# Kernel optimization log

Measured on AMD Instinct MI355X. Metric: run time of the kernel, lower is better.

The kernel has to match this reference:

```python
import jax, jax.numpy as jnp
import numpy as np

N, H, E = 50000, 128, 1600000

def setup_inputs() -> dict:
    key = jax.random.key(0)
    k1, k2, k3, k4 = jax.random.split(key, 4)
    h = jax.random.normal(k1, (N, H), dtype=jnp.float32)
    edge_index = jax.random.randint(k2, (2, E), 0, N, dtype=jnp.int64)
    # edge_scorer: Linear(2H, 1); node_scorer: Linear(H, 1)
    W_edge = jax.random.normal(k3, (2 * H, 1), dtype=jnp.float32) / np.sqrt(2 * H)
    b_edge = jnp.zeros((1,), dtype=jnp.float32)
    W_node = jax.random.normal(k4, (H, 1), dtype=jnp.float32) / np.sqrt(H)
    b_node = jnp.zeros((1,), dtype=jnp.float32)
    return {"h": h, "edge_index": edge_index, "W_edge": W_edge,
            "b_edge": b_edge, "W_node": W_node, "b_node": b_node}

def reference(h, edge_index, W_edge, b_edge, W_node, b_node):
    n = h.shape[0]
    src, dst = edge_index[0], edge_index[1]
    # cat([h[src], h[dst]]) @ W_edge == (h @ W_src)[src] + (h @ W_dst)[dst]
    # (same math as the torch module, avoids materializing the (E, 2H) concat)
    W_src, W_dst = W_edge[:h.shape[1]], W_edge[h.shape[1]:]
    s_src = (h @ W_src)[:, 0]            # (N,)
    s_dst = (h @ W_dst)[:, 0]            # (N,)
    edge_scores = s_src[src] + s_dst[dst] + b_edge[0]   # (E,)
    node_edge_score = jax.ops.segment_sum(edge_scores, dst, num_segments=n)
    node_self_score = (h @ W_node)[:, 0] + b_node[0]    # (N,)
    combined = node_edge_score + node_self_score
    return jax.nn.softmax(combined, axis=0)
```

## Files before the change

kernel.cpp:

```cpp
#include <hip/hip_runtime.h>
#include <math.h>


#define RANGE_BITS 14
#define RANGE_SIZE (1 << RANGE_BITS)
#define NCHUNKS 128
#define STAT_BLOCKS 256

typedef float vfloat4 __attribute__((ext_vector_type(4)));

__global__ __launch_bounds__(256) void node_scores_kernel(
    const float* __restrict__ h,
    const float* __restrict__ W_edge,
    const float* __restrict__ b_edge,
    const float* __restrict__ W_node,
    const float* __restrict__ b_node,
    float* __restrict__ s_src,
    float* __restrict__ t_dst,
    float* __restrict__ self_sc,
    float* __restrict__ acc,
    int N, int H)
{
    const int lane16 = threadIdx.x & 15;
    const int n = (blockIdx.x * blockDim.x + threadIdx.x) >> 4;
    if (n >= N) return;

    const float4* __restrict__ h4  = (const float4*)(h + (size_t)n * H);
    const float4* __restrict__ ws4 = (const float4*)(W_edge);
    const float4* __restrict__ wd4 = (const float4*)(W_edge + H);
    const float4* __restrict__ wn4 = (const float4*)(W_node);
    const int H4 = H >> 2;

    float ps = 0.0f, pd = 0.0f, pn = 0.0f;
    for (int i = lane16; i < H4; i += 16) {
        float4 hv = h4[i];
        float4 a = ws4[i], b = wd4[i], c = wn4[i];
        ps = fmaf(hv.x, a.x, fmaf(hv.y, a.y, fmaf(hv.z, a.z, fmaf(hv.w, a.w, ps))));
        pd = fmaf(hv.x, b.x, fmaf(hv.y, b.y, fmaf(hv.z, b.z, fmaf(hv.w, b.w, pd))));
        pn = fmaf(hv.x, c.x, fmaf(hv.y, c.y, fmaf(hv.z, c.z, fmaf(hv.w, c.w, pn))));
    }
    #pragma unroll
    for (int off = 8; off > 0; off >>= 1) {
        ps += __shfl_xor(ps, off, 64);
        pd += __shfl_xor(pd, off, 64);
        pn += __shfl_xor(pn, off, 64);
    }
    if (lane16 == 0) {
        float self = pn + b_node[0];
        s_src[n]   = ps;
        t_dst[n]   = pd + b_edge[0];
        self_sc[n] = self;
        acc[n]     = self;
    }
}

__global__ __launch_bounds__(1024) void edge_bin_kernel(
    const int* __restrict__ ei,
    const float* __restrict__ s_src,
    const float* __restrict__ t_dst,
    float* __restrict__ partials,
    int N, int E, int chunk, int vec_ok)
{
    __shared__ float hist[RANGE_SIZE];
    const int b  = blockIdx.x;
    const int r  = blockIdx.y;
    const int lo = r << RANGE_BITS;
    const int hi = min(lo + RANGE_SIZE, N);
    const unsigned span = (unsigned)(hi - lo);

    {
        vfloat4* __restrict__ hz = (vfloat4*)hist;
        const vfloat4 z = {0.0f, 0.0f, 0.0f, 0.0f};
        for (int i = threadIdx.x; i < (RANGE_SIZE >> 2); i += blockDim.x)
            hz[i] = z;
    }
    __syncthreads();

    const int e0 = b * chunk;
    const int e1 = min(e0 + chunk, E);
    if (e0 < e1) {
        if (vec_ok) {
            const int nvec = (e1 - e0) >> 2;
            const int4* __restrict__ dst4 = (const int4*)(ei + E + e0);
            const int4* __restrict__ src4 = (const int4*)(ei + e0);
            for (int i = threadIdx.x; i < nvec; i += blockDim.x) {
                int4 d = dst4[i];
                int4 s = src4[i];
                unsigned ux = (unsigned)(d.x - lo), uy = (unsigned)(d.y - lo);
                unsigned uz = (unsigned)(d.z - lo), uw = (unsigned)(d.w - lo);
                if (ux < span) atomicAdd(&hist[ux], s_src[s.x] + t_dst[d.x]);
                if (uy < span) atomicAdd(&hist[uy], s_src[s.y] + t_dst[d.y]);
                if (uz < span) atomicAdd(&hist[uz], s_src[s.z] + t_dst[d.z]);
                if (uw < span) atomicAdd(&hist[uw], s_src[s.w] + t_dst[d.w]);
            }
            for (int e = e0 + 4 * nvec + threadIdx.x; e < e1; e += blockDim.x) {
                int d = ei[E + e];
                unsigned u = (unsigned)(d - lo);
                if (u < span) atomicAdd(&hist[u], s_src[ei[e]] + t_dst[d]);
            }
        } else {
            for (int e = e0 + threadIdx.x; e < e1; e += blockDim.x) {
                int d = ei[E + e];
                unsigned u = (unsigned)(d - lo);
                if (u < span) atomicAdd(&hist[u], s_src[ei[e]] + t_dst[d]);
            }
        }
    }
    __syncthreads();

    float* __restrict__ outp = partials + (size_t)b * N + lo;
    const int len = hi - lo;
    if ((len & 3) == 0) {
        const int len4 = len >> 2;
        const vfloat4* __restrict__ h4 = (const vfloat4*)hist;
        vfloat4* __restrict__ o4 = (vfloat4*)outp;
        for (int i = threadIdx.x; i < len4; i += blockDim.x)
            __builtin_nontemporal_store(h4[i], &o4[i]);
    } else {
        for (int i = threadIdx.x; i < len; i += blockDim.x)
            __builtin_nontemporal_store(hist[i], &outp[i]);
    }
}

__global__ __launch_bounds__(256) void edge_accum_fallback_kernel(
    const int* __restrict__ ei,
    const float* __restrict__ s_src,
    const float* __restrict__ t_dst,
    float* __restrict__ acc,
    int E)
{
    int e = blockIdx.x * blockDim.x + threadIdx.x;
    if (e >= E) return;
    int s = ei[e];
    int d = ei[E + e];
    atomicAdd(&acc[d], s_src[s] + t_dst[d]);
}

__device__ __forceinline__ float blockReduceMaxB(float v) {
    __shared__ float sm[16];
    #pragma unroll
    for (int off = 32; off > 0; off >>= 1) v = fmaxf(v, __shfl_xor(v, off, 64));
    const int w = threadIdx.x >> 6, l = threadIdx.x & 63;
    const int nw = blockDim.x >> 6;
    if (l == 0) sm[w] = v;
    __syncthreads();
    float r = sm[0];
    for (int i = 1; i < nw; ++i) r = fmaxf(r, sm[i]);
    __syncthreads();
    return r;
}

__device__ __forceinline__ float blockReduceSumB(float v) {
    __shared__ float sm[16];
    #pragma unroll
    for (int off = 32; off > 0; off >>= 1) v += __shfl_xor(v, off, 64);
    const int w = threadIdx.x >> 6, l = threadIdx.x & 63;
    const int nw = blockDim.x >> 6;
    if (l == 0) sm[w] = v;
    __syncthreads();
    float r = 0.0f;
    for (int i = 0; i < nw; ++i) r += sm[i];
    __syncthreads();
    return r;
}

__global__ __launch_bounds__(256) void combine_stats_kernel(
    const float* __restrict__ self_sc,
    const float* __restrict__ partials,
    float* __restrict__ acc,
    float* __restrict__ red,
    int N, int B, int use_partials)
{
    float m = -INFINITY, l = 0.0f;
    for (int i = blockIdx.x * blockDim.x + threadIdx.x; i < N;
         i += gridDim.x * blockDim.x) {
        float v;
        if (use_partials) {
            float v0 = self_sc[i], v1 = 0.0f, v2 = 0.0f, v3 = 0.0f;
            int b = 0;
            for (; b + 4 <= B; b += 4) {
                v0 += __builtin_nontemporal_load(&partials[(size_t)(b + 0) * N + i]);
                v1 += __builtin_nontemporal_load(&partials[(size_t)(b + 1) * N + i]);
                v2 += __builtin_nontemporal_load(&partials[(size_t)(b + 2) * N + i]);
                v3 += __builtin_nontemporal_load(&partials[(size_t)(b + 3) * N + i]);
            }
            for (; b < B; ++b) v0 += partials[(size_t)b * N + i];
            v = (v0 + v1) + (v2 + v3);
            acc[i] = v;
        } else {
            v = acc[i];
        }
        float nm = fmaxf(m, v);
        l = l * __expf(m - nm) + __expf(v - nm);
        m = nm;
    }
    float mb = blockReduceMaxB(m);
    float ladj = (m == -INFINITY) ? 0.0f : l * __expf(m - mb);
    float lb = blockReduceSumB(ladj);
    if (threadIdx.x == 0) {
        red[blockIdx.x] = mb;
        red[STAT_BLOCKS + blockIdx.x] = lb;
    }
}

__global__ __launch_bounds__(256) void finalize_kernel(
    const float* __restrict__ acc,
    const float* __restrict__ red,
    float* __restrict__ out,
    int N)
{
    float m = red[threadIdx.x];
    float l = red[STAT_BLOCKS + threadIdx.x];
    float M = blockReduceMaxB(m);
    float L = blockReduceSumB(l * __expf(m - M));
    const float inv = 1.0f / L;

    int i = blockIdx.x * blockDim.x + threadIdx.x;
    if (i < N) out[i] = __expf(acc[i] - M) * inv;
}

extern "C" void kernel_launch(void* const* d_in, const int* in_sizes, int n_in,
                              void* d_out, int out_size, void* d_ws, size_t ws_size,
                              hipStream_t stream) {
    const float* h      = (const float*)d_in[0];
    const int*   ei     = (const int*)  d_in[1];
    const float* W_edge = (const float*)d_in[2];
    const float* b_edge = (const float*)d_in[3];
    const float* W_node = (const float*)d_in[4];
    const float* b_node = (const float*)d_in[5];

    const int H = in_sizes[2] / 2;
    const int N = in_sizes[0] / H;
    const int E = in_sizes[1] / 2;

    float* out      = (float*)d_out;
    float* ws       = (float*)d_ws;
    float* s_src    = ws;
    float* t_dst    = ws + (size_t)N;
    float* self_s   = ws + 2 * (size_t)N;
    float* acc      = ws + 3 * (size_t)N;
    float* red      = ws + 4 * (size_t)N;
    float* partials = red + 2 * STAT_BLOCKS;

    const size_t base_floats = 4 * (size_t)N + 2 * STAT_BLOCKS;
    int B = 0;
    if (ws_size / sizeof(float) > base_floats) {
        size_t avail = ws_size / sizeof(float) - base_floats;
        B = (int)(avail / (size_t)N);
    }
    if (B > NCHUNKS) B = NCHUNKS;
    const int R = (N + RANGE_SIZE - 1) >> RANGE_BITS;
    const int use_partials = (B >= 16) ? 1 : 0;

    {
        int threads = N * 16;
        int grid = (threads + 255) / 256;
        node_scores_kernel<<<grid, 256, 0, stream>>>(
            h, W_edge, b_edge, W_node, b_node,
            s_src, t_dst, self_s, acc, N, H);
    }
    if (use_partials) {
        int chunk = (((E + B - 1) / B) + 3) & ~3;
        int vec_ok = ((E & 3) == 0) ? 1 : 0;
        dim3 grid(B, R);
        edge_bin_kernel<<<grid, 1024, 0, stream>>>(
            ei, s_src, t_dst, partials, N, E, chunk, vec_ok);
    } else {
        int grid = (E + 255) / 256;
        edge_accum_fallback_kernel<<<grid, 256, 0, stream>>>(ei, s_src, t_dst, acc, E);
    }
    combine_stats_kernel<<<STAT_BLOCKS, 256, 0, stream>>>(
        self_s, partials, acc, red, N, B, use_partials);
    {
        int grid = (N + 255) / 256;
        finalize_kernel<<<grid, 256, 0, stream>>>(acc, red, out, N);
    }
}
```

Measured before the change: 123.5 us.

## Halve edge chunks and add swizzled 1D-grid edge binning kernel

```diff
diff --git a/kernel.cpp b/kernel.cpp
--- a/kernel.cpp
+++ b/kernel.cpp
@@ -4,7 +4,7 @@
 
 #define RANGE_BITS 14
 #define RANGE_SIZE (1 << RANGE_BITS)
-#define NCHUNKS 128
+#define NCHUNKS 64
 #define STAT_BLOCKS 256
 
 typedef float vfloat4 __attribute__((ext_vector_type(4)));
@@ -54,6 +54,94 @@
     }
 }
 
+__global__ __launch_bounds__(1024) void edge_bin_swz_kernel(
+    const int* __restrict__ ei,
+    const float* __restrict__ s_src,
+    const float* __restrict__ t_dst,
+    float* __restrict__ partials,
+    int N, int E, int chunk, int vec_ok)
+{
+    __shared__ float hist[RANGE_SIZE];
+    const int id = blockIdx.x;
+    const int g  = id & 7;
+    const int s  = id >> 3;
+    const int b  = (g << 3) | (s & 7);
+    const int r  = s >> 3;
+    const int lo = r << RANGE_BITS;
+    const int hi = min(lo + RANGE_SIZE, N);
+    const unsigned span = (unsigned)(hi - lo);
+
+    {
+        vfloat4* __restrict__ hz = (vfloat4*)hist;
+        const vfloat4 z = {0.0f, 0.0f, 0.0f, 0.0f};
+        for (int i = threadIdx.x; i < (RANGE_SIZE >> 2); i += blockDim.x)
+            hz[i] = z;
+    }
+    __syncthreads();
+
+    const int e0 = b * chunk;
+    const int e1 = min(e0 + chunk, E);
+    if (e0 < e1) {
+        if (vec_ok) {
+            const int nvec = (e1 - e0) >> 2;
+            const int4* __restrict__ dst4 = (const int4*)(ei + E + e0);
+            const int4* __restrict__ src4 = (const int4*)(ei + e0);
+            int i = threadIdx.x;
+            for (; i + (int)blockDim.x < nvec; i += 2 * blockDim.x) {
+                int4 da = dst4[i];
+                int4 db = dst4[i + blockDim.x];
+                int4 sa = src4[i];
+                int4 sb = src4[i + blockDim.x];
+                unsigned ax = (unsigned)(da.x - lo), ay = (unsigned)(da.y - lo);
+                unsigned az = (unsigned)(da.z - lo), aw = (unsigned)(da.w - lo);
+                if (ax < span) atomicAdd(&hist[ax], s_src[sa.x] + t_dst[da.x]);
+                if (ay < span) atomicAdd(&hist[ay], s_src[sa.y] + t_dst[da.y]);
+                if (az < span) atomicAdd(&hist[az], s_src[sa.z] + t_dst[da.z]);
+                if (aw < span) atomicAdd(&hist[aw], s_src[sa.w] + t_dst[da.w]);
+                unsigned bx = (unsigned)(db.x - lo), by = (unsigned)(db.y - lo);
+                unsigned bz = (unsigned)(db.z - lo), bw = (unsigned)(db.w - lo);
+                if (bx < span) atomicAdd(&hist[bx], s_src[sb.x] + t_dst[db.x]);
+                if (by < span) atomicAdd(&hist[by], s_src[sb.y] + t_dst[db.y]);
+                if (bz < span) atomicAdd(&hist[bz], s_src[sb.z] + t_dst[db.z]);
+                if (bw < span) atomicAdd(&hist[bw], s_src[sb.w] + t_dst[db.w]);
+            }
+            if (i < nvec) {
+                int4 da = dst4[i];
+                int4 sa = src4[i];
+                unsigned ax = (unsigned)(da.x - lo), ay = (unsigned)(da.y - lo);
+                unsigned az = (unsigned)(da.z - lo), aw = (unsigned)(da.w - lo);
+                if (ax < span) atomicAdd(&hist[ax], s_src[sa.x] + t_dst[da.x]);
+                if (ay < span) atomicAdd(&hist[ay], s_src[sa.y] + t_dst[da.y]);
+                if (az < span) atomicAdd(&hist[az], s_src[sa.z] + t_dst[da.z]);
+                if (aw < span) atomicAdd(&hist[aw], s_src[sa.w] + t_dst[da.w]);
+            }
+            for (int e = e0 + 4 * nvec + threadIdx.x; e < e1; e += blockDim.x) {
+                int d = ei[E + e];
+                unsigned u = (unsigned)(d - lo);
+                if (u < span) atomicAdd(&hist[u], s_src[ei[e]] + t_dst[d]);
+            }
+        } else {
+            for (int e = e0 + threadIdx.x; e < e1; e += blockDim.x) {
+                int d = ei[E + e];
+                unsigned u = (unsigned)(d - lo);
+                if (u < span) atomicAdd(&hist[u], s_src[ei[e]] + t_dst[d]);
+            }
+        }
+    }
+    __syncthreads();
+
+    float* __restrict__ outp = partials + (size_t)b * N + lo;
+    const int len = hi - lo;
+    if ((len & 3) == 0) {
+        const int len4 = len >> 2;
+        const vfloat4* __restrict__ h4 = (const vfloat4*)hist;
+        vfloat4* __restrict__ o4 = (vfloat4*)outp;
+        for (int i = threadIdx.x; i < len4; i += blockDim.x) o4[i] = h4[i];
+    } else {
+        for (int i = threadIdx.x; i < len; i += blockDim.x) outp[i] = hist[i];
+    }
+}
+
 __global__ __launch_bounds__(1024) void edge_bin_kernel(
     const int* __restrict__ ei,
     const float* __restrict__ s_src,
@@ -68,12 +156,7 @@
     const int hi = min(lo + RANGE_SIZE, N);
     const unsigned span = (unsigned)(hi - lo);
 
-    {
-        vfloat4* __restrict__ hz = (vfloat4*)hist;
-        const vfloat4 z = {0.0f, 0.0f, 0.0f, 0.0f};
-        for (int i = threadIdx.x; i < (RANGE_SIZE >> 2); i += blockDim.x)
-            hz[i] = z;
-    }
+    for (int i = threadIdx.x; i < RANGE_SIZE; i += blockDim.x) hist[i] = 0.0f;
     __syncthreads();
 
     const int e0 = b * chunk;
@@ -110,16 +193,7 @@
 
     float* __restrict__ outp = partials + (size_t)b * N + lo;
     const int len = hi - lo;
-    if ((len & 3) == 0) {
-        const int len4 = len >> 2;
-        const vfloat4* __restrict__ h4 = (const vfloat4*)hist;
-        vfloat4* __restrict__ o4 = (vfloat4*)outp;
-        for (int i = threadIdx.x; i < len4; i += blockDim.x)
-            __builtin_nontemporal_store(h4[i], &o4[i]);
-    } else {
-        for (int i = threadIdx.x; i < len; i += blockDim.x)
-            __builtin_nontemporal_store(hist[i], &outp[i]);
-    }
+    for (int i = threadIdx.x; i < len; i += blockDim.x) outp[i] = hist[i];
 }
 
 __global__ __launch_bounds__(256) void edge_accum_fallback_kernel(
@@ -179,10 +253,10 @@
             float v0 = self_sc[i], v1 = 0.0f, v2 = 0.0f, v3 = 0.0f;
             int b = 0;
             for (; b + 4 <= B; b += 4) {
-                v0 += __builtin_nontemporal_load(&partials[(size_t)(b + 0) * N + i]);
-                v1 += __builtin_nontemporal_load(&partials[(size_t)(b + 1) * N + i]);
-                v2 += __builtin_nontemporal_load(&partials[(size_t)(b + 2) * N + i]);
-                v3 += __builtin_nontemporal_load(&partials[(size_t)(b + 3) * N + i]);
+                v0 += partials[(size_t)(b + 0) * N + i];
+                v1 += partials[(size_t)(b + 1) * N + i];
+                v2 += partials[(size_t)(b + 2) * N + i];
+                v3 += partials[(size_t)(b + 3) * N + i];
             }
             for (; b < B; ++b) v0 += partials[(size_t)b * N + i];
             v = (v0 + v1) + (v2 + v3);
@@ -262,9 +336,14 @@
     if (use_partials) {
         int chunk = (((E + B - 1) / B) + 3) & ~3;
         int vec_ok = ((E & 3) == 0) ? 1 : 0;
-        dim3 grid(B, R);
-        edge_bin_kernel<<<grid, 1024, 0, stream>>>(
-            ei, s_src, t_dst, partials, N, E, chunk, vec_ok);
+        if (B == NCHUNKS && R == 4) {
+            edge_bin_swz_kernel<<<256, 1024, 0, stream>>>(
+                ei, s_src, t_dst, partials, N, E, chunk, vec_ok);
+        } else {
+            dim3 grid(B, R);
+            edge_bin_kernel<<<grid, 1024, 0, stream>>>(
+                ei, s_src, t_dst, partials, N, E, chunk, vec_ok);
+        }
     } else {
         int grid = (E + 255) / 256;
         edge_accum_fallback_kernel<<<grid, 256, 0, stream>>>(ei, s_src, t_dst, acc, E);
```

Result: faster. 112.7 us (-8.8%).
